# Kernel optimization log

Hardware: AMD Instinct MI355X
Metric: run time of the kernel (lower is better)

The kernel has to match this reference:

```python
import jax, jax.numpy as jnp
import numpy as np

B, C, W, H = 4, 256, 64, 64
DK = C // 8  # query/key channels


def setup_inputs() -> dict:
    key = jax.random.key(0)
    ks = jax.random.split(key, 7)
    x = jax.random.normal(ks[0], (B, C, W, H), dtype=jnp.float32)
    # conv1x1 weights stored as [out_ch, in_ch]
    Wq = jax.random.normal(ks[1], (DK, C), dtype=jnp.float32) / np.sqrt(C)
    bq = jnp.zeros((DK,), dtype=jnp.float32)
    Wk = jax.random.normal(ks[2], (DK, C), dtype=jnp.float32) / np.sqrt(C)
    bk = jnp.zeros((DK,), dtype=jnp.float32)
    Wv = jax.random.normal(ks[3], (C, C), dtype=jnp.float32) / np.sqrt(C)
    bv = jnp.zeros((C,), dtype=jnp.float32)
    gamma = jnp.zeros((1,), dtype=jnp.float32)
    return {"x": x, "Wq": Wq, "bq": bq, "Wk": Wk, "bk": bk,
            "Wv": Wv, "bv": bv, "gamma": gamma}


def reference(x, Wq, bq, Wk, bk, Wv, bv, gamma):
    b, c, w, h = x.shape
    n = w * h
    xf = x.reshape(b, c, n)                     # [B, C, N]
    # conv1x1 == channel matmul
    q = jnp.einsum('dc,bcn->bnd', Wq, xf) + bq  # [B, N, DK]
    k = jnp.einsum('dc,bcn->bdn', Wk, xf) + bk[None, :, None]  # [B, DK, N]
    energy = jnp.einsum('bnd,bdm->bnm', q, k)   # [B, N, N]
    attention = jax.nn.softmax(energy, axis=-1)
    v = jnp.einsum('dc,bcn->bdn', Wv, xf) + bv[None, :, None]  # [B, C, N]
    out = jnp.einsum('bdm,bnm->bdn', v, attention)              # [B, C, N]
    out = out.reshape(b, c, w, h)
    out = gamma * out + x
    return out, attention
```

## Files before the change

kernel.cpp:

```cpp
#include <hip/hip_runtime.h>
#include <hip/hip_bf16.h>

typedef __attribute__((ext_vector_type(8))) short bf16x8;
typedef __attribute__((ext_vector_type(4))) float f32x4;
typedef __attribute__((ext_vector_type(4))) unsigned int u32x4;
typedef __attribute__((ext_vector_type(2))) unsigned int u32x2;

#define B_SZ 4
#define C_SZ 256
#define N_SZ 4096
#define DK_SZ 32

#define WQB_OFF 0
#define WKB_OFF 8192
#define WVB_OFF 16384
#define QB_OFF  81920
#define KB_OFF  606208
#define VB_OFF  1130496

__device__ __forceinline__ short f2bf(float f) {
    union { float f; unsigned int u; } v; v.f = f;
    unsigned int r = v.u + 0x7fffu + ((v.u >> 16) & 1u);
    return (short)(r >> 16);
}

__device__ __forceinline__ float asf(unsigned int u) {
    union { unsigned int u; float f; } v; v.u = u;
    return v.f;
}

__device__ __forceinline__ unsigned int cvt_pk_bf16(float lo, float hi) {
    unsigned int r;
    asm volatile("v_cvt_pk_bf16_f32 %0, %1, %2" : "=v"(r) : "v"(lo), "v"(hi));
    return r;
}

__device__ __forceinline__ f32x4 mfma16(bf16x8 a, bf16x8 b, f32x4 c) {
    return __builtin_amdgcn_mfma_f32_16x16x32_bf16(a, b, c, 0, 0, 0);
}

__device__ __forceinline__ void gload_lds16(const void* g, void* l) {
    __builtin_amdgcn_global_load_lds((const __attribute__((address_space(1))) unsigned int*)g,
                                     (__attribute__((address_space(3))) unsigned int*)l, 16, 0, 0);
}

__device__ __forceinline__ void remap_block(int i, int& b, int& n0) {
    b = (i & 7) >> 1;
    n0 = (((i >> 3) << 1) | (i & 1)) * 64;
}

__global__ __launch_bounds__(256) void k_convw(const float* __restrict__ Wq,
                                               const float* __restrict__ Wk,
                                               const float* __restrict__ Wv,
                                               short* __restrict__ ws) {
    int i = blockIdx.x * 256 + threadIdx.x;
    if (i < 8192) {
        ws[WQB_OFF + i] = f2bf(Wq[i]);
        ws[WKB_OFF + i] = f2bf(Wk[i]);
    }
    ws[WVB_OFF + i] = f2bf(Wv[i]);
}

__global__ __launch_bounds__(256) void k_prep(const float* __restrict__ x,
                                              const float* __restrict__ bq,
                                              const float* __restrict__ bk,
                                              const float* __restrict__ bv,
                                              short* __restrict__ ws) {
    __shared__ short xsT[64][264];
    __shared__ short vt_s[64][258];

    int b, n0;
    remap_block(blockIdx.x, b, n0);
    const int t = threadIdx.x;
    const float* xb = x + (size_t)b * C_SZ * N_SZ;

    {
        int c0 = t >> 4, n4 = (t & 15) * 4;
#pragma unroll
        for (int i = 0; i < 16; i++) {
            int c = c0 + 16 * i;
            float4 v = *(const float4*)(xb + (size_t)c * N_SZ + n0 + n4);
            xsT[n4 + 0][c] = f2bf(v.x);
            xsT[n4 + 1][c] = f2bf(v.y);
            xsT[n4 + 2][c] = f2bf(v.z);
            xsT[n4 + 3][c] = f2bf(v.w);
        }
    }
    __syncthreads();

    const int w = t >> 6, l = t & 63;
    const int lr = l & 15, lk = l >> 4;

    bf16x8 af[8];
#pragma unroll
    for (int kk = 0; kk < 8; kk++)
        af[kk] = *(const bf16x8*)(&xsT[w * 16 + lr][kk * 32 + lk * 8]);

#pragma unroll
    for (int qk = 0; qk < 2; qk++) {
        const short* wb = ws + (qk ? WKB_OFF : WQB_OFF);
        const float* bias = qk ? bk : bq;
        short* outp = ws + (qk ? KB_OFF : QB_OFF) + (size_t)b * N_SZ * DK_SZ;
#pragma unroll
        for (int cf = 0; cf < 2; cf++) {
            f32x4 acc = {0.f, 0.f, 0.f, 0.f};
#pragma unroll
            for (int kk = 0; kk < 8; kk++) {
                bf16x8 bfr = *(const bf16x8*)(wb + (cf * 16 + lr) * 256 + kk * 32 + lk * 8);
                acc = mfma16(af[kk], bfr, acc);
            }
            float bias_v = bias[cf * 16 + lr];
#pragma unroll
            for (int r = 0; r < 4; r++) {
                int row = w * 16 + lk * 4 + r;
                outp[(size_t)(n0 + row) * DK_SZ + cf * 16 + lr] = f2bf(acc[r] + bias_v);
            }
        }
    }

#pragma unroll
    for (int cf = 0; cf < 16; cf++) {
        f32x4 acc = {0.f, 0.f, 0.f, 0.f};
#pragma unroll
        for (int kk = 0; kk < 8; kk++) {
            bf16x8 bfr = *(const bf16x8*)(ws + WVB_OFF + (cf * 16 + lr) * 256 + kk * 32 + lk * 8);
            acc = mfma16(af[kk], bfr, acc);
        }
        float bias_v = bv[cf * 16 + lr];
#pragma unroll
        for (int r = 0; r < 4; r++) {
            vt_s[w * 16 + lk * 4 + r][cf * 16 + lr] = f2bf(acc[r] + bias_v);
        }
    }
    __syncthreads();
    {
        short* vb = ws + VB_OFF + (size_t)b * C_SZ * N_SZ;
        int nn = t & 63;
#pragma unroll
        for (int i = 0; i < 64; i++) {
            int c = (t >> 6) + 4 * i;
            vb[(size_t)c * N_SZ + n0 + nn] = vt_s[nn][c];
        }
    }
}

__global__ __launch_bounds__(512, 1) void k_attn(const short* __restrict__ ws,
                                                 const float* __restrict__ x,
                                                 const float* __restrict__ gamma_p,
                                                 float* __restrict__ out) {
    __shared__ short v_lds[3][16384];
    __shared__ short k_lds[3][2304];
    __shared__ short p_lds[2][64][72];
    __shared__ float rsum_s[2][64];

    int b, n0;
    remap_block(blockIdx.x, b, n0);
    const int t = threadIdx.x, w = t >> 6, l = t & 63;
    const int rg = w & 3, ch = w >> 2;
    const int lr = l & 15, lk = l >> 4;

    const short* qb = ws + QB_OFF + (size_t)b * N_SZ * DK_SZ;
    const short* kb = ws + KB_OFF + (size_t)b * N_SZ * DK_SZ;
    const short* vb = ws + VB_OFF + (size_t)b * C_SZ * N_SZ;
    const char* kbb = (const char*)kb;

    bf16x8 qf = *(const bf16x8*)(qb + (size_t)(n0 + rg * 16 + lr) * DK_SZ + lk * 8);

    float rs = 0.f;
    for (int mt = 0; mt < 32; mt++) {
        int mb = ch * 2048 + mt * 64;
        bf16x8 kfa = *(const bf16x8*)(kb + (size_t)(mb + lr) * DK_SZ + lk * 8);
        bf16x8 kfb = *(const bf16x8*)(kb + (size_t)(mb + 16 + lr) * DK_SZ + lk * 8);
        bf16x8 kfc = *(const bf16x8*)(kb + (size_t)(mb + 32 + lr) * DK_SZ + lk * 8);
        bf16x8 kfd = *(const bf16x8*)(kb + (size_t)(mb + 48 + lr) * DK_SZ + lk * 8);
        f32x4 s0 = mfma16(kfa, qf, (f32x4){0.f, 0.f, 0.f, 0.f});
        f32x4 s1 = mfma16(kfb, qf, (f32x4){0.f, 0.f, 0.f, 0.f});
        f32x4 s2 = mfma16(kfc, qf, (f32x4){0.f, 0.f, 0.f, 0.f});
        f32x4 s3 = mfma16(kfd, qf, (f32x4){0.f, 0.f, 0.f, 0.f});
#pragma unroll
        for (int r = 0; r < 4; r++)
            rs += __expf(s0[r]) + __expf(s1[r]) + __expf(s2[r]) + __expf(s3[r]);
    }
    rs += __shfl_xor(rs, 16);
    rs += __shfl_xor(rs, 32);
    if (l < 16) rsum_s[ch][rg * 16 + l] = rs;
    __syncthreads();
    const float invp = 1.f / (rsum_s[0][rg * 16 + lr] + rsum_s[1][rg * 16 + lr]);

    float* attn_b = out + (size_t)B_SZ * C_SZ * N_SZ + (size_t)b * N_SZ * N_SZ;
    f32x4 O[4][4];
#pragma unroll
    for (int cf = 0; cf < 4; cf++)
#pragma unroll
        for (int rgi = 0; rgi < 4; rgi++) O[cf][rgi] = (f32x4){0.f, 0.f, 0.f, 0.f};

    const int krow = ch * 32 + lr;
    const int kswz = ((lk ^ ((lr >> 1) & 3)) << 4);
    const int aoff = rg * 8192 + lr * 128 + ((((ch << 2) + lk) ^ (lr & 7)) << 4);
    const int boff = lr * 144 + ch * 64 + lk * 16;

    bf16x8 kf0, kf1;

#define STAGE(tt, buf)                                                              \
    {                                                                               \
        const int krw = w * 8 + (l >> 2);                                           \
        const int ksl = (l & 3) ^ ((l >> 3) & 3);                                   \
        gload_lds16(kbb + (size_t)(tt) * 4096 + krw * 64 + ksl * 16,                \
                    (void*)&k_lds[buf][w * 256]);                                   \
        const int mb = (tt) * 64;                                                   \
        _Pragma("unroll")                                                           \
        for (int i = 0; i < 4; i++) {                                               \
            int c = w * 32 + i * 8 + (l >> 3);                                      \
            int j = l & 7;                                                          \
            const short* gp = vb + (size_t)c * N_SZ + mb + ((j ^ (c & 7)) << 3);    \
            gload_lds16(gp, (void*)&v_lds[buf][(w * 32 + i * 8) * 64]);             \
        }                                                                           \
    }

#define KREAD(tt)                                                                   \
    {                                                                               \
        const char* kl = (const char*)&k_lds[(tt) % 3][0];                          \
        kf0 = *(const bf16x8*)(kl + krow * 64 + kswz);                              \
        kf1 = *(const bf16x8*)(kl + krow * 64 + 1024 + kswz);                       \
    }

#define SCOMP_BODY(tt, pb)                                                          \
    {                                                                               \
        f32x4 s0 = mfma16(kf0, qf, (f32x4){0.f, 0.f, 0.f, 0.f});                    \
        f32x4 s1 = mfma16(kf1, qf, (f32x4){0.f, 0.f, 0.f, 0.f});                    \
        float e00 = __expf(s0[0]) * invp, e01 = __expf(s0[1]) * invp;               \
        float e02 = __expf(s0[2]) * invp, e03 = __expf(s0[3]) * invp;               \
        float e10 = __expf(s1[0]) * invp, e11 = __expf(s1[1]) * invp;               \
        float e12 = __expf(s1[2]) * invp, e13 = __expf(s1[3]) * invp;               \
        u32x2 pk0, pk1;                                                             \
        pk0[0] = cvt_pk_bf16(e00, e01); pk0[1] = cvt_pk_bf16(e02, e03);             \
        pk1[0] = cvt_pk_bf16(e10, e11); pk1[1] = cvt_pk_bf16(e12, e13);             \
        *(u32x2*)(&p_lds[pb][rg * 16 + lr][ch * 32 + lk * 4]) = pk0;                \
        *(u32x2*)(&p_lds[pb][rg * 16 + lr][ch * 32 + 16 + lk * 4]) = pk1;           \
    }

#define ASTORE(tt)                                                                  \
    {                                                                               \
        const int arow = w * 8 + (l >> 3);                                          \
        const char* pr = (const char*)&p_lds[(tt) & 1][arow][0];                    \
        u32x2 u0 = *(const u32x2*)(pr + (l & 7) * 8);                               \
        u32x2 u1 = *(const u32x2*)(pr + 64 + (l & 7) * 8);                          \
        f32x4 f0, f1;                                                               \
        f0[0] = asf(u0[0] << 16); f0[1] = asf(u0[0] & 0xffff0000u);                 \
        f0[2] = asf(u0[1] << 16); f0[3] = asf(u0[1] & 0xffff0000u);                 \
        f1[0] = asf(u1[0] << 16); f1[1] = asf(u1[0] & 0xffff0000u);                 \
        f1[2] = asf(u1[1] << 16); f1[3] = asf(u1[1] & 0xffff0000u);                 \
        float* dst = attn_b + (size_t)(n0 + arow) * N_SZ + (tt) * 64 + (l & 7) * 4; \
        __builtin_nontemporal_store(f0, (f32x4*)dst);                               \
        __builtin_nontemporal_store(f1, (f32x4*)(dst + 32));                        \
    }

    STAGE(0, 0);
    STAGE(1, 1);
    __builtin_amdgcn_sched_barrier(0);
    asm volatile("s_waitcnt vmcnt(5)" ::: "memory");
    __builtin_amdgcn_sched_barrier(0);
    __builtin_amdgcn_s_barrier();
    KREAD(0);
    SCOMP_BODY(0, 0);

    for (int mt = 0; mt < 64; mt++) {
        asm volatile("s_waitcnt vmcnt(2) lgkmcnt(0)" ::: "memory");
        __builtin_amdgcn_sched_barrier(0);
        __builtin_amdgcn_s_barrier();
        __builtin_amdgcn_sched_barrier(0);
        const int cur = mt & 1;
        if (mt < 63) KREAD(mt + 1);
        if (mt < 62) STAGE(mt + 2, (mt + 2) % 3);
        __builtin_amdgcn_sched_barrier(0);
        if (mt < 63) SCOMP_BODY(mt + 1, cur ^ 1);
        __builtin_amdgcn_sched_barrier(0);
        ASTORE(mt);
        __builtin_amdgcn_sched_barrier(0);
        const char* vbase = (const char*)&v_lds[mt % 3][0];
        const char* pbase = (const char*)&p_lds[cur][0][0];
        bf16x8 Afr[4], Bfr[4];
#pragma unroll
        for (int cf = 0; cf < 4; cf++)
            Afr[cf] = *(const bf16x8*)(vbase + cf * 2048 + aoff);
#pragma unroll
        for (int rgi = 0; rgi < 4; rgi++)
            Bfr[rgi] = *(const bf16x8*)(pbase + rgi * 2304 + boff);
#pragma unroll
        for (int cf = 0; cf < 4; cf++)
#pragma unroll
            for (int rgi = 0; rgi < 4; rgi++)
                O[cf][rgi] = mfma16(Afr[cf], Bfr[rgi], O[cf][rgi]);
    }
#undef STAGE
#undef KREAD
#undef SCOMP_BODY
#undef ASTORE

    __syncthreads();
    float* o_red = (float*)&v_lds[0][0];
    const int RSTRIDE = 4360;
    if (ch == 1) {
#pragma unroll
        for (int cf = 0; cf < 4; cf++)
#pragma unroll
            for (int rgi = 0; rgi < 4; rgi++)
#pragma unroll
                for (int r = 0; r < 4; r++)
                    o_red[rgi * RSTRIDE + (rg * 64 + cf * 16 + 4 * lk + r) * 17 + lr] = O[cf][rgi][r];
    }
    __syncthreads();
    if (ch == 0) {
#pragma unroll
        for (int cf = 0; cf < 4; cf++)
#pragma unroll
            for (int rgi = 0; rgi < 4; rgi++)
#pragma unroll
                for (int r = 0; r < 4; r++) {
                    int idx = rgi * RSTRIDE + (rg * 64 + cf * 16 + 4 * lk + r) * 17 + lr;
                    o_red[idx] += O[cf][rgi][r];
                }
    }
    __syncthreads();
    {
        const float g = gamma_p[0];
        const float* xb = x + (size_t)b * C_SZ * N_SZ;
        float* ob = out + (size_t)b * C_SZ * N_SZ;
        int nn = t & 63;
        int c0 = t >> 6;
        int rbase = (nn >> 4) * RSTRIDE + (nn & 15);
#pragma unroll
        for (int i = 0; i < 32; i++) {
            int c = c0 + 8 * i;
            size_t idx = (size_t)c * N_SZ + n0 + nn;
            ob[idx] = g * o_red[rbase + c * 17] + xb[idx];
        }
    }
}

extern "C" void kernel_launch(void* const* d_in, const int* in_sizes, int n_in,
                              void* d_out, int out_size, void* d_ws, size_t ws_size,
                              hipStream_t stream) {
    const float* x     = (const float*)d_in[0];
    const float* Wq    = (const float*)d_in[1];
    const float* bq    = (const float*)d_in[2];
    const float* Wk    = (const float*)d_in[3];
    const float* bk    = (const float*)d_in[4];
    const float* Wv    = (const float*)d_in[5];
    const float* bv    = (const float*)d_in[6];
    const float* gamma = (const float*)d_in[7];
    short* ws = (short*)d_ws;
    float* out = (float*)d_out;

    hipLaunchKernelGGL(k_convw, dim3(256), dim3(256), 0, stream, Wq, Wk, Wv, ws);
    hipLaunchKernelGGL(k_prep, dim3(256), dim3(256), 0, stream, x, bq, bk, bv, ws);
    hipLaunchKernelGGL(k_attn, dim3(256), dim3(512), 0, stream, ws, x, gamma, out);
}
```

Before: 138.0 us.

## Load V and K fragments directly to registers with tiled V layout

Stores V in a tile-contiguous layout (per 64-column block, C×64) so the attention kernel can load MFMA A-fragments straight from global memory into registers. This drops the LDS staging of V and K via global_load_lds. The main loop now handles two tiles per iteration with register double-buffering and a four-slot P buffer, which halves the number of barriers. The cost is more register pressure and exposed global load latency, and the LDS footprint shrinks.

```diff
diff --git a/kernel.cpp b/kernel.cpp
--- a/kernel.cpp
+++ b/kernel.cpp
@@ -37,11 +37,6 @@
 
 __device__ __forceinline__ f32x4 mfma16(bf16x8 a, bf16x8 b, f32x4 c) {
     return __builtin_amdgcn_mfma_f32_16x16x32_bf16(a, b, c, 0, 0, 0);
-}
-
-__device__ __forceinline__ void gload_lds16(const void* g, void* l) {
-    __builtin_amdgcn_global_load_lds((const __attribute__((address_space(1))) unsigned int*)g,
-                                     (__attribute__((address_space(3))) unsigned int*)l, 16, 0, 0);
 }
 
 __device__ __forceinline__ void remap_block(int i, int& b, int& n0) {
@@ -134,12 +129,12 @@
     }
     __syncthreads();
     {
-        short* vb = ws + VB_OFF + (size_t)b * C_SZ * N_SZ;
+        short* vt = ws + VB_OFF + (size_t)b * C_SZ * N_SZ + (size_t)(n0 >> 6) * (C_SZ * 64);
         int nn = t & 63;
 #pragma unroll
         for (int i = 0; i < 64; i++) {
             int c = (t >> 6) + 4 * i;
-            vb[(size_t)c * N_SZ + n0 + nn] = vt_s[nn][c];
+            vt[c * 64 + nn] = vt_s[nn][c];
         }
     }
 }
@@ -148,10 +143,9 @@
                                                  const float* __restrict__ x,
                                                  const float* __restrict__ gamma_p,
                                                  float* __restrict__ out) {
-    __shared__ short v_lds[3][16384];
-    __shared__ short k_lds[3][2304];
-    __shared__ short p_lds[2][64][72];
-    __shared__ float rsum_s[2][64];
+    __shared__ __align__(16) char smem[69888];
+    short (*p_lds)[64][72] = (short(*)[64][72])smem;
+    float* rsum_s = (float*)(smem + 36864);
 
     int b, n0;
     remap_block(blockIdx.x, b, n0);
@@ -161,12 +155,12 @@
 
     const short* qb = ws + QB_OFF + (size_t)b * N_SZ * DK_SZ;
     const short* kb = ws + KB_OFF + (size_t)b * N_SZ * DK_SZ;
-    const short* vb = ws + VB_OFF + (size_t)b * C_SZ * N_SZ;
-    const char* kbb = (const char*)kb;
+    const short* vb2 = ws + VB_OFF + (size_t)b * C_SZ * N_SZ;
 
     bf16x8 qf = *(const bf16x8*)(qb + (size_t)(n0 + rg * 16 + lr) * DK_SZ + lk * 8);
 
     float rs = 0.f;
+#pragma unroll 2
     for (int mt = 0; mt < 32; mt++) {
         int mb = ch * 2048 + mt * 64;
         bf16x8 kfa = *(const bf16x8*)(kb + (size_t)(mb + lr) * DK_SZ + lk * 8);
@@ -183,9 +177,9 @@
     }
     rs += __shfl_xor(rs, 16);
     rs += __shfl_xor(rs, 32);
-    if (l < 16) rsum_s[ch][rg * 16 + l] = rs;
-    __syncthreads();
-    const float invp = 1.f / (rsum_s[0][rg * 16 + lr] + rsum_s[1][rg * 16 + lr]);
+    if (l < 16) rsum_s[ch * 64 + rg * 16 + l] = rs;
+    __syncthreads();
+    const float invp = 1.f / (rsum_s[rg * 16 + lr] + rsum_s[64 + rg * 16 + lr]);
 
     float* attn_b = out + (size_t)B_SZ * C_SZ * N_SZ + (size_t)b * N_SZ * N_SZ;
     f32x4 O[4][4];
@@ -194,40 +188,28 @@
 #pragma unroll
         for (int rgi = 0; rgi < 4; rgi++) O[cf][rgi] = (f32x4){0.f, 0.f, 0.f, 0.f};
 
-    const int krow = ch * 32 + lr;
-    const int kswz = ((lk ^ ((lr >> 1) & 3)) << 4);
-    const int aoff = rg * 8192 + lr * 128 + ((((ch << 2) + lk) ^ (lr & 7)) << 4);
     const int boff = lr * 144 + ch * 64 + lk * 16;
 
-    bf16x8 kf0, kf1;
-
-#define STAGE(tt, buf)                                                              \
-    {                                                                               \
-        const int krw = w * 8 + (l >> 2);                                           \
-        const int ksl = (l & 3) ^ ((l >> 3) & 3);                                   \
-        gload_lds16(kbb + (size_t)(tt) * 4096 + krw * 64 + ksl * 16,                \
-                    (void*)&k_lds[buf][w * 256]);                                   \
-        const int mb = (tt) * 64;                                                   \
+#define VLOAD(tt, vr)                                                               \
+    {                                                                               \
+        const short* vt = vb2 + (size_t)(tt) * (C_SZ * 64);                         \
         _Pragma("unroll")                                                           \
-        for (int i = 0; i < 4; i++) {                                               \
-            int c = w * 32 + i * 8 + (l >> 3);                                      \
-            int j = l & 7;                                                          \
-            const short* gp = vb + (size_t)c * N_SZ + mb + ((j ^ (c & 7)) << 3);    \
-            gload_lds16(gp, (void*)&v_lds[buf][(w * 32 + i * 8) * 64]);             \
-        }                                                                           \
-    }
-
-#define KREAD(tt)                                                                   \
-    {                                                                               \
-        const char* kl = (const char*)&k_lds[(tt) % 3][0];                          \
-        kf0 = *(const bf16x8*)(kl + krow * 64 + kswz);                              \
-        kf1 = *(const bf16x8*)(kl + krow * 64 + 1024 + kswz);                       \
-    }
-
-#define SCOMP_BODY(tt, pb)                                                          \
-    {                                                                               \
-        f32x4 s0 = mfma16(kf0, qf, (f32x4){0.f, 0.f, 0.f, 0.f});                    \
-        f32x4 s1 = mfma16(kf1, qf, (f32x4){0.f, 0.f, 0.f, 0.f});                    \
+        for (int cf = 0; cf < 4; cf++)                                              \
+            vr[cf] = *(const bf16x8*)(vt + (rg * 64 + cf * 16 + lr) * 64            \
+                                      + ch * 32 + lk * 8);                          \
+    }
+
+#define KLOAD(tt, k0, k1)                                                           \
+    {                                                                               \
+        const int mb = (tt) * 64 + ch * 32;                                         \
+        k0 = *(const bf16x8*)(kb + (size_t)(mb + lr) * DK_SZ + lk * 8);             \
+        k1 = *(const bf16x8*)(kb + (size_t)(mb + 16 + lr) * DK_SZ + lk * 8);        \
+    }
+
+#define SCOMP(tt, k0, k1)                                                           \
+    {                                                                               \
+        f32x4 s0 = mfma16(k0, qf, (f32x4){0.f, 0.f, 0.f, 0.f});                     \
+        f32x4 s1 = mfma16(k1, qf, (f32x4){0.f, 0.f, 0.f, 0.f});                     \
         float e00 = __expf(s0[0]) * invp, e01 = __expf(s0[1]) * invp;               \
         float e02 = __expf(s0[2]) * invp, e03 = __expf(s0[3]) * invp;               \
         float e10 = __expf(s1[0]) * invp, e11 = __expf(s1[1]) * invp;               \
@@ -235,14 +217,14 @@
         u32x2 pk0, pk1;                                                             \
         pk0[0] = cvt_pk_bf16(e00, e01); pk0[1] = cvt_pk_bf16(e02, e03);             \
         pk1[0] = cvt_pk_bf16(e10, e11); pk1[1] = cvt_pk_bf16(e12, e13);             \
-        *(u32x2*)(&p_lds[pb][rg * 16 + lr][ch * 32 + lk * 4]) = pk0;                \
-        *(u32x2*)(&p_lds[pb][rg * 16 + lr][ch * 32 + 16 + lk * 4]) = pk1;           \
+        *(u32x2*)(&p_lds[(tt) & 3][rg * 16 + lr][ch * 32 + lk * 4]) = pk0;          \
+        *(u32x2*)(&p_lds[(tt) & 3][rg * 16 + lr][ch * 32 + 16 + lk * 4]) = pk1;     \
     }
 
 #define ASTORE(tt)                                                                  \
     {                                                                               \
         const int arow = w * 8 + (l >> 3);                                          \
-        const char* pr = (const char*)&p_lds[(tt) & 1][arow][0];                    \
+        const char* pr = (const char*)&p_lds[(tt) & 3][arow][0];                    \
         u32x2 u0 = *(const u32x2*)(pr + (l & 7) * 8);                               \
         u32x2 u1 = *(const u32x2*)(pr + 64 + (l & 7) * 8);                          \
         f32x4 f0, f1;                                                               \
@@ -255,50 +237,60 @@
         __builtin_nontemporal_store(f1, (f32x4*)(dst + 32));                        \
     }
 
-    STAGE(0, 0);
-    STAGE(1, 1);
+#define PVOP(tt, vr)                                                                \
+    {                                                                               \
+        const char* pbase = (const char*)&p_lds[(tt) & 3][0][0];                    \
+        bf16x8 Bfr[4];                                                              \
+        _Pragma("unroll")                                                           \
+        for (int rgi = 0; rgi < 4; rgi++)                                           \
+            Bfr[rgi] = *(const bf16x8*)(pbase + rgi * 2304 + boff);                 \
+        _Pragma("unroll")                                                           \
+        for (int cf = 0; cf < 4; cf++)                                              \
+            _Pragma("unroll")                                                       \
+            for (int rgi = 0; rgi < 4; rgi++)                                       \
+                O[cf][rgi] = mfma16(vr[cf], Bfr[rgi], O[cf][rgi]);                  \
+    }
+
+#define FITER(f, CV0, CV1, CK00, CK01, CK10, CK11, NV0, NV1, NK00, NK01, NK10, NK11) \
+    {                                                                               \
+        if ((f) < 31) { VLOAD(2 * (f) + 2, NV0); VLOAD(2 * (f) + 3, NV1); }         \
+        if ((f) < 30) { KLOAD(2 * (f) + 4, NK00, NK01); KLOAD(2 * (f) + 5, NK10, NK11); } \
+        __builtin_amdgcn_sched_barrier(0);                                          \
+        if ((f) < 31) { SCOMP(2 * (f) + 2, CK00, CK01); SCOMP(2 * (f) + 3, CK10, CK11); } \
+        __builtin_amdgcn_sched_barrier(0);                                          \
+        ASTORE(2 * (f)); ASTORE(2 * (f) + 1);                                       \
+        PVOP(2 * (f), CV0); PVOP(2 * (f) + 1, CV1);                                 \
+        asm volatile("s_waitcnt lgkmcnt(0)" ::: "memory");                          \
+        __builtin_amdgcn_sched_barrier(0);                                          \
+        __builtin_amdgcn_s_barrier();                                               \
+        __builtin_amdgcn_sched_barrier(0);                                          \
+    }
+
+    bf16x8 vA0[4], vA1[4], vB0[4], vB1[4];
+    bf16x8 kA00, kA01, kA10, kA11, kB00, kB01, kB10, kB11;
+
+    VLOAD(0, vA0); VLOAD(1, vA1);
+    KLOAD(2, kA00, kA01); KLOAD(3, kA10, kA11);
+    KLOAD(0, kB00, kB01); KLOAD(1, kB10, kB11);
     __builtin_amdgcn_sched_barrier(0);
-    asm volatile("s_waitcnt vmcnt(5)" ::: "memory");
+    SCOMP(0, kB00, kB01); SCOMP(1, kB10, kB11);
+    asm volatile("s_waitcnt lgkmcnt(0)" ::: "memory");
+    __builtin_amdgcn_s_barrier();
     __builtin_amdgcn_sched_barrier(0);
-    __builtin_amdgcn_s_barrier();
-    KREAD(0);
-    SCOMP_BODY(0, 0);
-
-    for (int mt = 0; mt < 64; mt++) {
-        asm volatile("s_waitcnt vmcnt(2) lgkmcnt(0)" ::: "memory");
-        __builtin_amdgcn_sched_barrier(0);
-        __builtin_amdgcn_s_barrier();
-        __builtin_amdgcn_sched_barrier(0);
-        const int cur = mt & 1;
-        if (mt < 63) KREAD(mt + 1);
-        if (mt < 62) STAGE(mt + 2, (mt + 2) % 3);
-        __builtin_amdgcn_sched_barrier(0);
-        if (mt < 63) SCOMP_BODY(mt + 1, cur ^ 1);
-        __builtin_amdgcn_sched_barrier(0);
-        ASTORE(mt);
-        __builtin_amdgcn_sched_barrier(0);
-        const char* vbase = (const char*)&v_lds[mt % 3][0];
-        const char* pbase = (const char*)&p_lds[cur][0][0];
-        bf16x8 Afr[4], Bfr[4];
-#pragma unroll
-        for (int cf = 0; cf < 4; cf++)
-            Afr[cf] = *(const bf16x8*)(vbase + cf * 2048 + aoff);
-#pragma unroll
-        for (int rgi = 0; rgi < 4; rgi++)
-            Bfr[rgi] = *(const bf16x8*)(pbase + rgi * 2304 + boff);
-#pragma unroll
-        for (int cf = 0; cf < 4; cf++)
-#pragma unroll
-            for (int rgi = 0; rgi < 4; rgi++)
-                O[cf][rgi] = mfma16(Afr[cf], Bfr[rgi], O[cf][rgi]);
-    }
-#undef STAGE
-#undef KREAD
-#undef SCOMP_BODY
+
+    for (int f = 0; f < 32; f += 2) {
+        FITER(f, vA0, vA1, kA00, kA01, kA10, kA11, vB0, vB1, kB00, kB01, kB10, kB11);
+        FITER(f + 1, vB0, vB1, kB00, kB01, kB10, kB11, vA0, vA1, kA00, kA01, kA10, kA11);
+    }
+#undef VLOAD
+#undef KLOAD
+#undef SCOMP
 #undef ASTORE
-
-    __syncthreads();
-    float* o_red = (float*)&v_lds[0][0];
+#undef PVOP
+#undef FITER
+
+    __syncthreads();
+    float* o_red = (float*)smem;
     const int RSTRIDE = 4360;
     if (ch == 1) {
 #pragma unroll
```

Result: slower. 149.0 us (+8.0%).
